# Performance work log

Hardware: AMD Instinct MI355X
Metric: run time of the kernel (lower is better)

Reference implementation:

```python
import jax, jax.numpy as jnp
import numpy as np

H = 8        # num_heads
D = 64       # qkv_dim
E = 512      # embed_dim = H*D
MS = 16      # ms_hidden_dim


def setup_inputs() -> dict:
    key = jax.random.key(0)
    ks = jax.random.split(key, 12)
    b, r, c = 4, 512, 512
    row_emb = jax.random.normal(ks[0], (b, r, E), dtype=jnp.float32)
    col_emb = jax.random.normal(ks[1], (b, c, E), dtype=jnp.float32)
    cost_mat = jax.random.uniform(ks[2], (b, r, c), dtype=jnp.float32)
    attn_mask = jax.random.randint(ks[3], (b, H, r, c), 0, 2) > 0
    s = 1.0 / np.sqrt(E)
    Wq = jax.random.uniform(ks[4], (H * D, E), minval=-s, maxval=s)
    Wk = jax.random.uniform(ks[5], (H * D, E), minval=-s, maxval=s)
    Wv = jax.random.uniform(ks[6], (H * D, E), minval=-s, maxval=s)
    Wout = jax.random.uniform(ks[7], (E, E), minval=-s, maxval=s)
    m1 = np.sqrt(0.5)
    m2 = np.sqrt(1.0 / MS)
    Wmix1 = jax.random.uniform(ks[8], (H * MS, 2 * H), minval=-m1, maxval=m1)
    Wmix2 = jax.random.uniform(ks[9], (H, H * MS), minval=-m2, maxval=m2)
    return {"row_emb": row_emb, "col_emb": col_emb, "cost_mat": cost_mat,
            "attn_mask": attn_mask, "Wq": Wq, "Wk": Wk, "Wv": Wv,
            "Wmix1": Wmix1, "Wmix2": Wmix2, "Wout": Wout}


def reference(row_emb, col_emb, cost_mat, attn_mask, Wq, Wk, Wv, Wmix1, Wmix2, Wout):
    b, r, _ = row_emb.shape
    c = col_emb.shape[1]
    norm = 1.0 / jnp.sqrt(jnp.asarray(D, row_emb.dtype))
    # projections -> [b, h, s, d]
    q = (row_emb @ Wq.T).reshape(b, r, H, D).transpose(0, 2, 1, 3)
    k = (col_emb @ Wk.T).reshape(b, c, H, D).transpose(0, 2, 1, 3)
    v = (col_emb @ Wv.T).reshape(b, c, H, D).transpose(0, 2, 1, 3)
    dot = norm * jnp.einsum('bhrd,bhcd->bhrc', q, k)            # [b,h,r,c]
    cost = jnp.broadcast_to(cost_mat[:, None, :, :], dot.shape)  # [b,h,r,c]
    # stack then rearrange 'b h r c s -> b r c (h s)' (h major, s minor)
    two = jnp.stack([dot, cost], axis=-1)                        # [b,h,r,c,2]
    two = two.transpose(0, 2, 3, 1, 4).reshape(b, r, c, 2 * H)
    hid = jax.nn.relu(two @ Wmix1.T)                             # [b,r,c,H*MS]
    ms = hid @ Wmix2.T                                           # [b,r,c,H]
    logits = ms.transpose(0, 3, 1, 2)                            # [b,h,r,c]
    # mask handling: rows that are fully masked become fully unmasked
    all_masked = jnp.all(attn_mask, axis=-1, keepdims=True)
    mask = jnp.where(all_masked, False, attn_mask)
    logits = jnp.where(mask, -jnp.inf, logits)
    weights = jax.nn.softmax(logits, axis=-1)
    out = jnp.einsum('bhrc,bhcd->bhrd', weights, v)              # [b,h,r,d]
    out = out.transpose(0, 2, 1, 3).reshape(b, r, H * D)         # b s (h d)
    return out @ Wout.T
```

## Files before the change

### kernel.cpp

```cpp
#include <hip/hip_runtime.h>
#include <math.h>

typedef __attribute__((ext_vector_type(8))) short bf16x8;
typedef __attribute__((ext_vector_type(4))) float f32x4;
typedef unsigned short ushort_t;

static __device__ inline unsigned short f2bf(float f) {
    union { float f; unsigned u; } v; v.f = f;
    unsigned r = v.u + 0x7fff + ((v.u >> 16) & 1);
    return (unsigned short)(r >> 16);
}

#if defined(__has_builtin)
#  if __has_builtin(__builtin_amdgcn_cvt_pk_bf16_f32)
#    define HAVE_PK_BF16 1
#  endif
#endif

static __device__ inline unsigned pk2bf(float a, float b) {
#ifdef HAVE_PK_BF16
    auto r = __builtin_amdgcn_cvt_pk_bf16_f32(a, b);
    unsigned u; __builtin_memcpy(&u, &r, 4);
    return u;
#else
    return (unsigned)f2bf(a) | ((unsigned)f2bf(b) << 16);
#endif
}

__global__ __launch_bounds__(256) void convert_all(const float* __restrict__ a0,
                                                   const float* __restrict__ a1,
                                                   const float* __restrict__ a2,
                                                   const float* __restrict__ a3,
                                                   const float* __restrict__ a4,
                                                   const float* __restrict__ a5,
                                                   ushort_t* __restrict__ dst) {
    const size_t e = ((size_t)blockIdx.x * 256 + threadIdx.x) * 4;
    const float* src; size_t off;
    if      (e < 1048576) { src = a0; off = 0; }
    else if (e < 2097152) { src = a1; off = 1048576; }
    else if (e < 2359296) { src = a2; off = 2097152; }
    else if (e < 2621440) { src = a3; off = 2359296; }
    else if (e < 2883584) { src = a4; off = 2621440; }
    else                  { src = a5; off = 2883584; }
    const float4 v = *(const float4*)(src + (e - off));
    uint2 o; o.x = pk2bf(v.x, v.y); o.y = pk2bf(v.z, v.w);
    *(uint2*)(dst + e) = o;
}

__global__ __launch_bounds__(256) void gemm_qkv(const ushort_t* __restrict__ rowb,
                                                const ushort_t* __restrict__ colb,
                                                const ushort_t* __restrict__ Wqb,
                                                const ushort_t* __restrict__ Wkb,
                                                const ushort_t* __restrict__ Wvb,
                                                ushort_t* __restrict__ Qb,
                                                ushort_t* __restrict__ Kb,
                                                ushort_t* __restrict__ Vt) {
    const int z = blockIdx.z;
    const ushort_t* A = (z == 0) ? rowb : colb;
    const ushort_t* B = (z == 0) ? Wqb : (z == 1) ? Wkb : Wvb;

    const int t    = threadIdx.x;
    const int w    = t >> 6;
    const int lane = t & 63;
    const int quad = lane >> 4;
    const int sl   = lane & 15;
    const int m0 = blockIdx.x * 64 + (w >> 1) * 32;
    const int n0 = blockIdx.y * 64 + (w & 1) * 32;

    f32x4 acc[2][2] = {};

    for (int k0 = 0; k0 < 512; k0 += 32) {
        bf16x8 a[2], b[2];
#pragma unroll
        for (int rs = 0; rs < 2; ++rs)
            a[rs] = *(const bf16x8*)(A + (size_t)(m0 + rs * 16 + sl) * 512 + k0 + quad * 8);
#pragma unroll
        for (int cs = 0; cs < 2; ++cs)
            b[cs] = *(const bf16x8*)(B + (size_t)(n0 + cs * 16 + sl) * 512 + k0 + quad * 8);
#pragma unroll
        for (int rs = 0; rs < 2; ++rs)
#pragma unroll
            for (int cs = 0; cs < 2; ++cs)
                acc[rs][cs] = __builtin_amdgcn_mfma_f32_16x16x32_bf16(a[rs], b[cs], acc[rs][cs], 0, 0, 0);
    }

#pragma unroll
    for (int rs = 0; rs < 2; ++rs)
#pragma unroll
        for (int cs = 0; cs < 2; ++cs) {
            const int n = n0 + cs * 16 + sl;
            if (z == 2) {
                const int mb   = m0 + rs * 16 + quad * 4;
                const int bidx = mb >> 9, c = mb & 511;
                const int h = n >> 6, d = n & 63;
                ushort4 o;
                o.x = f2bf(acc[rs][cs][0]); o.y = f2bf(acc[rs][cs][1]);
                o.z = f2bf(acc[rs][cs][2]); o.w = f2bf(acc[rs][cs][3]);
                *(ushort4*)(Vt + (size_t)(((bidx * 8 + h) * 64 + d)) * 512 + c) = o;
            } else {
                ushort_t* C = (z == 0) ? Qb : Kb;
#pragma unroll
                for (int reg = 0; reg < 4; ++reg) {
                    const int m = m0 + rs * 16 + quad * 4 + reg;
                    C[(size_t)m * 512 + n] = f2bf(acc[rs][cs][reg]);
                }
            }
        }
}

__global__ __launch_bounds__(256) void gemm_out(const ushort_t* __restrict__ A,
                                                const ushort_t* __restrict__ B,
                                                float* __restrict__ C) {
    const int t    = threadIdx.x;
    const int w    = t >> 6;
    const int lane = t & 63;
    const int quad = lane >> 4;
    const int sl   = lane & 15;
    const int m0 = blockIdx.x * 64 + (w >> 1) * 32;
    const int n0 = blockIdx.y * 64 + (w & 1) * 32;

    f32x4 acc[2][2] = {};

    for (int k0 = 0; k0 < 512; k0 += 32) {
        bf16x8 a[2], b[2];
#pragma unroll
        for (int rs = 0; rs < 2; ++rs)
            a[rs] = *(const bf16x8*)(A + (size_t)(m0 + rs * 16 + sl) * 512 + k0 + quad * 8);
#pragma unroll
        for (int cs = 0; cs < 2; ++cs)
            b[cs] = *(const bf16x8*)(B + (size_t)(n0 + cs * 16 + sl) * 512 + k0 + quad * 8);
#pragma unroll
        for (int rs = 0; rs < 2; ++rs)
#pragma unroll
            for (int cs = 0; cs < 2; ++cs)
                acc[rs][cs] = __builtin_amdgcn_mfma_f32_16x16x32_bf16(a[rs], b[cs], acc[rs][cs], 0, 0, 0);
    }

#pragma unroll
    for (int rs = 0; rs < 2; ++rs)
#pragma unroll
        for (int cs = 0; cs < 2; ++cs) {
            const int n = n0 + cs * 16 + sl;
#pragma unroll
            for (int reg = 0; reg < 4; ++reg) {
                const int m = m0 + rs * 16 + quad * 4 + reg;
                C[(size_t)m * 512 + n] = acc[rs][cs][reg];
            }
        }
}

__global__ __launch_bounds__(512) void dot_mlp_v4(const ushort_t* __restrict__ Qb,
                                                  const ushort_t* __restrict__ Kb,
                                                  const float* __restrict__ cost,
                                                  const float* __restrict__ W1,
                                                  const float* __restrict__ W2,
                                                  float* __restrict__ logits) {
    __shared__ ushort_t Xs[1024 * 18];
    __shared__ ushort_t hidS[8 * 16 * 36];
    __shared__ ushort_t W1fs[128 * 16];
    __shared__ ushort_t W2ss[8 * 128];

    const int b  = blockIdx.z;
    const int r0 = blockIdx.y * 32;
    const int c0 = blockIdx.x * 32;
    const int t    = threadIdx.x;
    const int w    = t >> 6;
    const int lane = t & 63;
    const int quad = lane >> 4;
    const int sl   = lane & 15;

    const bf16x8 zf = {0, 0, 0, 0, 0, 0, 0, 0};

    if (t < 128) {
        float s = 0.f;
#pragma unroll
        for (int h = 0; h < 8; ++h) {
            W1fs[t * 16 + h] = f2bf(W1[t * 16 + 2 * h]);
            s += W1[t * 16 + 2 * h + 1];
        }
        W1fs[t * 16 + 8] = f2bf(s);
#pragma unroll
        for (int k = 9; k < 16; ++k) W1fs[t * 16 + k] = 0;
    }
#pragma unroll
    for (int i = 0; i < 2; ++i) W2ss[t + i * 512] = f2bf(W2[t + i * 512]);

#pragma unroll
    for (int i = 0; i < 2; ++i) {
        const int cell = t + i * 512;
        const int rl = cell >> 5, cl = cell & 31;
        unsigned* base = (unsigned*)(Xs + cell * 18 + 8);
        base[0] = (unsigned)f2bf(cost[((size_t)b * 512 + r0 + rl) * 512 + c0 + cl]);
        base[1] = 0; base[2] = 0; base[3] = 0; base[4] = 0;
    }

    {
        const int h = w;
        bf16x8 af[2][2], bfr[2][2];
#pragma unroll
        for (int rs = 0; rs < 2; ++rs)
#pragma unroll
            for (int ks = 0; ks < 2; ++ks)
                af[rs][ks] = *(const bf16x8*)(Qb +
                    ((size_t)(b * 512 + r0 + rs * 16 + sl) * 512 + h * 64 + ks * 32 + quad * 8));
#pragma unroll
        for (int cs = 0; cs < 2; ++cs)
#pragma unroll
            for (int ks = 0; ks < 2; ++ks)
                bfr[cs][ks] = *(const bf16x8*)(Kb +
                    ((size_t)(b * 512 + c0 + cs * 16 + sl) * 512 + h * 64 + ks * 32 + quad * 8));
#pragma unroll
        for (int rs = 0; rs < 2; ++rs)
#pragma unroll
            for (int cs = 0; cs < 2; ++cs) {
                f32x4 acc = {0.f, 0.f, 0.f, 0.f};
                acc = __builtin_amdgcn_mfma_f32_16x16x32_bf16(af[rs][0], bfr[cs][0], acc, 0, 0, 0);
                acc = __builtin_amdgcn_mfma_f32_16x16x32_bf16(af[rs][1], bfr[cs][1], acc, 0, 0, 0);
#pragma unroll
                for (int reg = 0; reg < 4; ++reg) {
                    const int cell = (rs * 16 + quad * 4 + reg) * 32 + cs * 16 + sl;
                    Xs[cell * 18 + h] = f2bf(acc[reg] * 0.125f);
                }
            }
    }

    __syncthreads();

    bf16x8 bw1[8];
#pragma unroll
    for (int nt = 0; nt < 8; ++nt)
        bw1[nt] = (quad < 2) ? *(const bf16x8*)&W1fs[(nt * 16 + sl) * 16 + quad * 8] : zf;
    bf16x8 bw2[4];
#pragma unroll
    for (int ks = 0; ks < 4; ++ks) {
        union { ushort_t s[8]; bf16x8 v; } tu;
#pragma unroll
        for (int i = 0; i < 8; ++i) {
            const int p  = quad * 8 + i;
            const int jc = (p >> 1) | ((p & 1) << 4);
            tu.s[i] = (sl < 8) ? W2ss[sl * 128 + ks * 32 + jc] : (ushort_t)0;
        }
        bw2[ks] = tu.v;
    }

    ushort_t* hidW = hidS + w * (16 * 36);

#pragma unroll
    for (int mt = 0; mt < 8; ++mt) {
        const int gmt = w * 8 + mt;
        const int cb  = gmt * 16;

        bf16x8 a1 = zf;
        if (quad < 2) {
            const unsigned* xr = (const unsigned*)Xs + (size_t)(cb + sl) * 9 + quad * 4;
            union { unsigned u[4]; bf16x8 v; } tmp;
            tmp.u[0] = xr[0]; tmp.u[1] = xr[1]; tmp.u[2] = xr[2]; tmp.u[3] = xr[3];
            a1 = tmp.v;
        }

        f32x4 acc2 = {0.f, 0.f, 0.f, 0.f};
#pragma unroll
        for (int ks = 0; ks < 4; ++ks) {
            f32x4 z = {0.f, 0.f, 0.f, 0.f};
            const f32x4 h0 = __builtin_amdgcn_mfma_f32_16x16x32_bf16(a1, bw1[2 * ks],     z, 0, 0, 0);
            const f32x4 h1 = __builtin_amdgcn_mfma_f32_16x16x32_bf16(a1, bw1[2 * ks + 1], z, 0, 0, 0);
#pragma unroll
            for (int rp = 0; rp < 4; ++rp)
                ((unsigned*)hidW)[(quad * 4 + rp) * 18 + sl] =
                    pk2bf(fmaxf(h0[rp], 0.f), fmaxf(h1[rp], 0.f));
            union { uint2 u2[2]; bf16x8 v; } tu;
            const ushort_t* hp = hidW + sl * 36 + quad * 8;
            tu.u2[0] = *(const uint2*)hp;
            tu.u2[1] = *(const uint2*)(hp + 4);
            acc2 = __builtin_amdgcn_mfma_f32_16x16x32_bf16(tu.v, bw2[ks], acc2, 0, 0, 0);
        }

        if (sl < 8) {
            const int r = r0 + (gmt >> 1);
            const int cbase = c0 + (gmt & 1) * 16 + quad * 4;
            float4 o; o.x = acc2[0]; o.y = acc2[1]; o.z = acc2[2]; o.w = acc2[3];
            *(float4*)&logits[((size_t)(b * 8 + sl) * 512 + r) * 512 + cbase] = o;
        }
    }
}

__global__ __launch_bounds__(256) void softmax_pv(const float* __restrict__ logits,
                                                  const int* __restrict__ mask,
                                                  const ushort_t* __restrict__ Vt,
                                                  ushort_t* __restrict__ Aout) {
    __shared__ ushort_t Ps[32 * 520];

    const int t    = threadIdx.x;
    const int w    = t >> 6;
    const int lane = t & 63;
    const int quad = lane >> 4;
    const int sl   = lane & 15;
    const int rt = blockIdx.x;
    const int bh = blockIdx.y;
    const int r0 = rt * 32;

#pragma unroll
    for (int rr = 0; rr < 8; ++rr) {
        const int row = w * 8 + rr;
        const float* lp = logits + ((size_t)bh * 512 + r0 + row) * 512;
        const int*   mp = mask   + ((size_t)bh * 512 + r0 + row) * 512;

        float v[8]; int m[8]; int allm = 1;
#pragma unroll
        for (int i = 0; i < 8; ++i) {
            v[i] = lp[lane + i * 64];
            m[i] = mp[lane + i * 64];
            allm &= (m[i] != 0);
        }
        const bool all_masked = (__all(allm) != 0);

        float mx = -__builtin_inff();
#pragma unroll
        for (int i = 0; i < 8; ++i) {
            const bool keep = all_masked || (m[i] == 0);
            if (keep) mx = fmaxf(mx, v[i]);
        }
#pragma unroll
        for (int s = 32; s > 0; s >>= 1) mx = fmaxf(mx, __shfl_xor(mx, s, 64));

        float e[8]; float sum = 0.f;
#pragma unroll
        for (int i = 0; i < 8; ++i) {
            const bool keep = all_masked || (m[i] == 0);
            e[i] = keep ? __expf(v[i] - mx) : 0.f;
            sum += e[i];
        }
#pragma unroll
        for (int s = 32; s > 0; s >>= 1) sum += __shfl_xor(sum, s, 64);

        const float inv = 1.f / sum;
#pragma unroll
        for (int i = 0; i < 8; ++i)
            Ps[row * 520 + lane + i * 64] = f2bf(e[i] * inv);
    }

    __syncthreads();

    const int mt  = w >> 1;
    const int n0w = (w & 1) * 32;
    const ushort_t* vb = Vt + (size_t)bh * 64 * 512;

    f32x4 acc[2] = {};
    for (int ks = 0; ks < 16; ++ks) {
        union { uint2 u2[2]; bf16x8 v; } ta;
        const ushort_t* pp = Ps + (size_t)(mt * 16 + sl) * 520 + ks * 32 + quad * 8;
        ta.u2[0] = *(const uint2*)pp;
        ta.u2[1] = *(const uint2*)(pp + 4);
        bf16x8 bv[2];
#pragma unroll
        for (int cn = 0; cn < 2; ++cn)
            bv[cn] = *(const bf16x8*)(vb + (size_t)(n0w + cn * 16 + sl) * 512 + ks * 32 + quad * 8);
#pragma unroll
        for (int cn = 0; cn < 2; ++cn)
            acc[cn] = __builtin_amdgcn_mfma_f32_16x16x32_bf16(ta.v, bv[cn], acc[cn], 0, 0, 0);
    }

    const int bidx = bh >> 3, h = bh & 7;
    ushort_t* Cb = Aout + (size_t)bidx * 512 * 512 + h * 64;
#pragma unroll
    for (int cn = 0; cn < 2; ++cn) {
        const int n = n0w + cn * 16 + sl;
#pragma unroll
        for (int reg = 0; reg < 4; ++reg) {
            const int m = r0 + mt * 16 + quad * 4 + reg;
            Cb[(size_t)m * 512 + n] = f2bf(acc[cn][reg]);
        }
    }
}

extern "C" void kernel_launch(void* const* d_in, const int* in_sizes, int n_in,
                              void* d_out, int out_size, void* d_ws, size_t ws_size,
                              hipStream_t stream) {
    const float* row_emb = (const float*)d_in[0];
    const float* col_emb = (const float*)d_in[1];
    const float* cost    = (const float*)d_in[2];
    const int*   mask    = (const int*)d_in[3];
    const float* Wq      = (const float*)d_in[4];
    const float* Wk      = (const float*)d_in[5];
    const float* Wv      = (const float*)d_in[6];
    const float* Wmix1   = (const float*)d_in[7];
    const float* Wmix2   = (const float*)d_in[8];
    const float* Wout    = (const float*)d_in[9];
    float* out = (float*)d_out;

    char* ws = (char*)d_ws;
    const size_t MB = (size_t)1 << 20;
    ushort_t* convDst = (ushort_t*)ws;
    ushort_t* rowb  = (ushort_t*)(ws);
    ushort_t* colb  = (ushort_t*)(ws + 2 * MB);
    ushort_t* Wqb   = (ushort_t*)(ws + 4 * MB);
    ushort_t* Wkb   = (ushort_t*)(ws + 4 * MB + 512 * 1024);
    ushort_t* Wvb   = (ushort_t*)(ws + 5 * MB);
    ushort_t* Woutb = (ushort_t*)(ws + 5 * MB + 512 * 1024);
    ushort_t* Qb    = (ushort_t*)(ws + 6 * MB);
    ushort_t* Kb    = (ushort_t*)(ws + 8 * MB);
    ushort_t* Vt    = (ushort_t*)(ws + 10 * MB);
    ushort_t* Aoutb = (ushort_t*)(ws + 12 * MB);
    float* logitsBuf = (float*)(ws + 40 * MB);

    convert_all<<<3072, 256, 0, stream>>>(row_emb, col_emb, Wq, Wk, Wv, Wout, convDst);

    gemm_qkv<<<dim3(32, 8, 3), 256, 0, stream>>>(rowb, colb, Wqb, Wkb, Wvb, Qb, Kb, Vt);

    dot_mlp_v4<<<dim3(16, 16, 4), 512, 0, stream>>>(Qb, Kb, cost, Wmix1, Wmix2, logitsBuf);

    softmax_pv<<<dim3(16, 32), 256, 0, stream>>>(logitsBuf, mask, Vt, Aoutb);

    gemm_out<<<dim3(32, 8), 256, 0, stream>>>(Aoutb, Woutb, out);
}
```

Baseline: 186.8 us.

## Fuse fp32-to-bf16 conversion into GEMM loads and rebalance dot and softmax tiling

Removes the separate convert_all pass: the QKV and output GEMMs now load fp32 inputs and weights and pack them to bf16 in registers. This saves one launch and a full write and re-read of converted data, but each GEMM block now reads twice the bytes with no reuse. dot_mlp now has each wave handle two heads for one 16-row slice and write packed bf16 pairs to shared memory. softmax_pv now uses 16-row tiles, doubling the grid and halving shared memory, at the cost of more redundant V reads.

```diff
diff --git a/kernel.cpp b/kernel.cpp
--- a/kernel.cpp
+++ b/kernel.cpp
@@ -27,37 +27,26 @@
 #endif
 }
 
-__global__ __launch_bounds__(256) void convert_all(const float* __restrict__ a0,
-                                                   const float* __restrict__ a1,
-                                                   const float* __restrict__ a2,
-                                                   const float* __restrict__ a3,
-                                                   const float* __restrict__ a4,
-                                                   const float* __restrict__ a5,
-                                                   ushort_t* __restrict__ dst) {
-    const size_t e = ((size_t)blockIdx.x * 256 + threadIdx.x) * 4;
-    const float* src; size_t off;
-    if      (e < 1048576) { src = a0; off = 0; }
-    else if (e < 2097152) { src = a1; off = 1048576; }
-    else if (e < 2359296) { src = a2; off = 2097152; }
-    else if (e < 2621440) { src = a3; off = 2359296; }
-    else if (e < 2883584) { src = a4; off = 2621440; }
-    else                  { src = a5; off = 2883584; }
-    const float4 v = *(const float4*)(src + (e - off));
-    uint2 o; o.x = pk2bf(v.x, v.y); o.y = pk2bf(v.z, v.w);
-    *(uint2*)(dst + e) = o;
-}
-
-__global__ __launch_bounds__(256) void gemm_qkv(const ushort_t* __restrict__ rowb,
-                                                const ushort_t* __restrict__ colb,
-                                                const ushort_t* __restrict__ Wqb,
-                                                const ushort_t* __restrict__ Wkb,
-                                                const ushort_t* __restrict__ Wvb,
+static __device__ inline bf16x8 ld8f32_bf16(const float* __restrict__ p) {
+    const float4 v0 = *(const float4*)p;
+    const float4 v1 = *(const float4*)(p + 4);
+    union { unsigned u[4]; bf16x8 v; } t;
+    t.u[0] = pk2bf(v0.x, v0.y); t.u[1] = pk2bf(v0.z, v0.w);
+    t.u[2] = pk2bf(v1.x, v1.y); t.u[3] = pk2bf(v1.z, v1.w);
+    return t.v;
+}
+
+__global__ __launch_bounds__(256) void gemm_qkv(const float* __restrict__ rowe,
+                                                const float* __restrict__ cole,
+                                                const float* __restrict__ Wq,
+                                                const float* __restrict__ Wk,
+                                                const float* __restrict__ Wv,
                                                 ushort_t* __restrict__ Qb,
                                                 ushort_t* __restrict__ Kb,
                                                 ushort_t* __restrict__ Vt) {
     const int z = blockIdx.z;
-    const ushort_t* A = (z == 0) ? rowb : colb;
-    const ushort_t* B = (z == 0) ? Wqb : (z == 1) ? Wkb : Wvb;
+    const float* A = (z == 0) ? rowe : cole;
+    const float* B = (z == 0) ? Wq : (z == 1) ? Wk : Wv;
 
     const int t    = threadIdx.x;
     const int w    = t >> 6;
@@ -73,10 +62,10 @@
         bf16x8 a[2], b[2];
 #pragma unroll
         for (int rs = 0; rs < 2; ++rs)
-            a[rs] = *(const bf16x8*)(A + (size_t)(m0 + rs * 16 + sl) * 512 + k0 + quad * 8);
+            a[rs] = ld8f32_bf16(A + (size_t)(m0 + rs * 16 + sl) * 512 + k0 + quad * 8);
 #pragma unroll
         for (int cs = 0; cs < 2; ++cs)
-            b[cs] = *(const bf16x8*)(B + (size_t)(n0 + cs * 16 + sl) * 512 + k0 + quad * 8);
+            b[cs] = ld8f32_bf16(B + (size_t)(n0 + cs * 16 + sl) * 512 + k0 + quad * 8);
 #pragma unroll
         for (int rs = 0; rs < 2; ++rs)
 #pragma unroll
@@ -109,7 +98,7 @@
 }
 
 __global__ __launch_bounds__(256) void gemm_out(const ushort_t* __restrict__ A,
-                                                const ushort_t* __restrict__ B,
+                                                const float* __restrict__ B,
                                                 float* __restrict__ C) {
     const int t    = threadIdx.x;
     const int w    = t >> 6;
@@ -128,7 +117,7 @@
             a[rs] = *(const bf16x8*)(A + (size_t)(m0 + rs * 16 + sl) * 512 + k0 + quad * 8);
 #pragma unroll
         for (int cs = 0; cs < 2; ++cs)
-            b[cs] = *(const bf16x8*)(B + (size_t)(n0 + cs * 16 + sl) * 512 + k0 + quad * 8);
+            b[cs] = ld8f32_bf16(B + (size_t)(n0 + cs * 16 + sl) * 512 + k0 + quad * 8);
 #pragma unroll
         for (int rs = 0; rs < 2; ++rs)
 #pragma unroll
@@ -149,7 +138,7 @@
         }
 }
 
-__global__ __launch_bounds__(512) void dot_mlp_v4(const ushort_t* __restrict__ Qb,
+__global__ __launch_bounds__(512) void dot_mlp_v5(const ushort_t* __restrict__ Qb,
                                                   const ushort_t* __restrict__ Kb,
                                                   const float* __restrict__ cost,
                                                   const float* __restrict__ W1,
@@ -195,32 +184,38 @@
     }
 
     {
-        const int h = w;
-        bf16x8 af[2][2], bfr[2][2];
-#pragma unroll
-        for (int rs = 0; rs < 2; ++rs)
-#pragma unroll
-            for (int ks = 0; ks < 2; ++ks)
-                af[rs][ks] = *(const bf16x8*)(Qb +
-                    ((size_t)(b * 512 + r0 + rs * 16 + sl) * 512 + h * 64 + ks * 32 + quad * 8));
-#pragma unroll
-        for (int cs = 0; cs < 2; ++cs)
-#pragma unroll
-            for (int ks = 0; ks < 2; ++ks)
-                bfr[cs][ks] = *(const bf16x8*)(Kb +
-                    ((size_t)(b * 512 + c0 + cs * 16 + sl) * 512 + h * 64 + ks * 32 + quad * 8));
-#pragma unroll
-        for (int rs = 0; rs < 2; ++rs)
+        const int hp = w & 3;
+        const int h0 = hp * 2;
+        const int rs = w >> 2;
+        bf16x8 af[2][2], bfr[2][2][2];
+#pragma unroll
+        for (int hh = 0; hh < 2; ++hh)
+#pragma unroll
+            for (int ks = 0; ks < 2; ++ks) {
+                af[hh][ks] = *(const bf16x8*)(Qb +
+                    ((size_t)(b * 512 + r0 + rs * 16 + sl) * 512 + (h0 + hh) * 64 + ks * 32 + quad * 8));
+#pragma unroll
+                for (int cs = 0; cs < 2; ++cs)
+                    bfr[hh][cs][ks] = *(const bf16x8*)(Kb +
+                        ((size_t)(b * 512 + c0 + cs * 16 + sl) * 512 + (h0 + hh) * 64 + ks * 32 + quad * 8));
+            }
+        f32x4 dacc[2][2];
+#pragma unroll
+        for (int hh = 0; hh < 2; ++hh)
 #pragma unroll
             for (int cs = 0; cs < 2; ++cs) {
                 f32x4 acc = {0.f, 0.f, 0.f, 0.f};
-                acc = __builtin_amdgcn_mfma_f32_16x16x32_bf16(af[rs][0], bfr[cs][0], acc, 0, 0, 0);
-                acc = __builtin_amdgcn_mfma_f32_16x16x32_bf16(af[rs][1], bfr[cs][1], acc, 0, 0, 0);
-#pragma unroll
-                for (int reg = 0; reg < 4; ++reg) {
-                    const int cell = (rs * 16 + quad * 4 + reg) * 32 + cs * 16 + sl;
-                    Xs[cell * 18 + h] = f2bf(acc[reg] * 0.125f);
-                }
+                acc = __builtin_amdgcn_mfma_f32_16x16x32_bf16(af[hh][0], bfr[hh][cs][0], acc, 0, 0, 0);
+                acc = __builtin_amdgcn_mfma_f32_16x16x32_bf16(af[hh][1], bfr[hh][cs][1], acc, 0, 0, 0);
+                dacc[hh][cs] = acc;
+            }
+#pragma unroll
+        for (int cs = 0; cs < 2; ++cs)
+#pragma unroll
+            for (int reg = 0; reg < 4; ++reg) {
+                const int cell = (rs * 16 + quad * 4 + reg) * 32 + cs * 16 + sl;
+                ((unsigned*)Xs)[cell * 9 + hp] =
+                    pk2bf(dacc[0][cs][reg] * 0.125f, dacc[1][cs][reg] * 0.125f);
             }
     }
 
@@ -269,9 +264,9 @@
                 ((unsigned*)hidW)[(quad * 4 + rp) * 18 + sl] =
                     pk2bf(fmaxf(h0[rp], 0.f), fmaxf(h1[rp], 0.f));
             union { uint2 u2[2]; bf16x8 v; } tu;
-            const ushort_t* hp = hidW + sl * 36 + quad * 8;
-            tu.u2[0] = *(const uint2*)hp;
-            tu.u2[1] = *(const uint2*)(hp + 4);
+            const ushort_t* hp2 = hidW + sl * 36 + quad * 8;
+            tu.u2[0] = *(const uint2*)hp2;
+            tu.u2[1] = *(const uint2*)(hp2 + 4);
             acc2 = __builtin_amdgcn_mfma_f32_16x16x32_bf16(tu.v, bw2[ks], acc2, 0, 0, 0);
         }
 
@@ -288,7 +283,7 @@
                                                   const int* __restrict__ mask,
                                                   const ushort_t* __restrict__ Vt,
                                                   ushort_t* __restrict__ Aout) {
-    __shared__ ushort_t Ps[32 * 520];
+    __shared__ ushort_t Ps[16 * 520];
 
     const int t    = threadIdx.x;
     const int w    = t >> 6;
@@ -297,11 +292,11 @@
     const int sl   = lane & 15;
     const int rt = blockIdx.x;
     const int bh = blockIdx.y;
-    const int r0 = rt * 32;
-
-#pragma unroll
-    for (int rr = 0; rr < 8; ++rr) {
-        const int row = w * 8 + rr;
+    const int r0 = rt * 16;
+
+#pragma unroll
+    for (int rr = 0; rr < 4; ++rr) {
+        const int row = w * 4 + rr;
         const float* lp = logits + ((size_t)bh * 512 + r0 + row) * 512;
         const int*   mp = mask   + ((size_t)bh * 512 + r0 + row) * 512;
 
@@ -341,35 +336,26 @@
 
     __syncthreads();
 
-    const int mt  = w >> 1;
-    const int n0w = (w & 1) * 32;
+    const int n0w = w * 16;
     const ushort_t* vb = Vt + (size_t)bh * 64 * 512;
 
-    f32x4 acc[2] = {};
+    f32x4 acc = {0.f, 0.f, 0.f, 0.f};
     for (int ks = 0; ks < 16; ++ks) {
         union { uint2 u2[2]; bf16x8 v; } ta;
-        const ushort_t* pp = Ps + (size_t)(mt * 16 + sl) * 520 + ks * 32 + quad * 8;
+        const ushort_t* pp = Ps + (size_t)sl * 520 + ks * 32 + quad * 8;
         ta.u2[0] = *(const uint2*)pp;
         ta.u2[1] = *(const uint2*)(pp + 4);
-        bf16x8 bv[2];
-#pragma unroll
-        for (int cn = 0; cn < 2; ++cn)
-            bv[cn] = *(const bf16x8*)(vb + (size_t)(n0w + cn * 16 + sl) * 512 + ks * 32 + quad * 8);
-#pragma unroll
-        for (int cn = 0; cn < 2; ++cn)
-            acc[cn] = __builtin_amdgcn_mfma_f32_16x16x32_bf16(ta.v, bv[cn], acc[cn], 0, 0, 0);
+        const bf16x8 bv = *(const bf16x8*)(vb + (size_t)(n0w + sl) * 512 + ks * 32 + quad * 8);
+        acc = __builtin_amdgcn_mfma_f32_16x16x32_bf16(ta.v, bv, acc, 0, 0, 0);
     }
 
     const int bidx = bh >> 3, h = bh & 7;
     ushort_t* Cb = Aout + (size_t)bidx * 512 * 512 + h * 64;
-#pragma unroll
-    for (int cn = 0; cn < 2; ++cn) {
-        const int n = n0w + cn * 16 + sl;
-#pragma unroll
-        for (int reg = 0; reg < 4; ++reg) {
-            const int m = r0 + mt * 16 + quad * 4 + reg;
-            Cb[(size_t)m * 512 + n] = f2bf(acc[cn][reg]);
-        }
+    const int n = n0w + sl;
+#pragma unroll
+    for (int reg = 0; reg < 4; ++reg) {
+        const int m = r0 + quad * 4 + reg;
+        Cb[(size_t)m * 512 + n] = f2bf(acc[reg]);
     }
 }
 
@@ -390,26 +376,17 @@
 
     char* ws = (char*)d_ws;
     const size_t MB = (size_t)1 << 20;
-    ushort_t* convDst = (ushort_t*)ws;
-    ushort_t* rowb  = (ushort_t*)(ws);
-    ushort_t* colb  = (ushort_t*)(ws + 2 * MB);
-    ushort_t* Wqb   = (ushort_t*)(ws + 4 * MB);
-    ushort_t* Wkb   = (ushort_t*)(ws + 4 * MB + 512 * 1024);
-    ushort_t* Wvb   = (ushort_t*)(ws + 5 * MB);
-    ushort_t* Woutb = (ushort_t*)(ws + 5 * MB + 512 * 1024);
-    ushort_t* Qb    = (ushort_t*)(ws + 6 * MB);
-    ushort_t* Kb    = (ushort_t*)(ws + 8 * MB);
-    ushort_t* Vt    = (ushort_t*)(ws + 10 * MB);
-    ushort_t* Aoutb = (ushort_t*)(ws + 12 * MB);
-    float* logitsBuf = (float*)(ws + 40 * MB);
-
-    convert_all<<<3072, 256, 0, stream>>>(row_emb, col_emb, Wq, Wk, Wv, Wout, convDst);
-
-    gemm_qkv<<<dim3(32, 8, 3), 256, 0, stream>>>(rowb, colb, Wqb, Wkb, Wvb, Qb, Kb, Vt);
-
-    dot_mlp_v4<<<dim3(16, 16, 4), 512, 0, stream>>>(Qb, Kb, cost, Wmix1, Wmix2, logitsBuf);
-
-    softmax_pv<<<dim3(16, 32), 256, 0, stream>>>(logitsBuf, mask, Vt, Aoutb);
-
-    gemm_out<<<dim3(32, 8), 256, 0, stream>>>(Aoutb, Woutb, out);
-}
+    ushort_t* Qb    = (ushort_t*)(ws);
+    ushort_t* Kb    = (ushort_t*)(ws + 2 * MB);
+    ushort_t* Vt    = (ushort_t*)(ws + 4 * MB);
+    ushort_t* Aoutb = (ushort_t*)(ws + 6 * MB);
+    float* logitsBuf = (float*)(ws + 8 * MB);
+
+    gemm_qkv<<<dim3(32, 8, 3), 256, 0, stream>>>(row_emb, col_emb, Wq, Wk, Wv, Qb, Kb, Vt);
+
+    dot_mlp_v5<<<dim3(16, 16, 4), 512, 0, stream>>>(Qb, Kb, cost, Wmix1, Wmix2, logitsBuf);
+
+    softmax_pv<<<dim3(32, 32), 256, 0, stream>>>(logitsBuf, mask, Vt, Aoutb);
+
+    gemm_out<<<dim3(32, 8), 256, 0, stream>>>(Aoutb, Wout, out);
+}
```

New measurement: 219.0 us. +17.2%, slower.
